# Kernel tuning notes

Measured on AMD Instinct MI355X. Metric: run time of the kernel, lower is better.

Reference implementation:

```python
import jax, jax.numpy as jnp
import numpy as np

B, N, CIN, COUT = 32, 2048, 64, 128
BN_EPS = 1e-5
ADJ_EPS = 1e-6


def setup_inputs() -> dict:
    key = jax.random.key(0)
    k0, k1, k2 = jax.random.split(key, 3)
    x = jax.random.normal(k0, (B, N, CIN), dtype=jnp.float32)
    # adjacency: nonnegative weights, like an attention/affinity graph
    A = jax.random.uniform(k1, (B, N, N), dtype=jnp.float32)
    # 1x1 conv == pointwise linear over channels
    W = jax.random.normal(k2, (COUT, CIN), dtype=jnp.float32) * 0.05
    b = jnp.zeros((COUT,), dtype=jnp.float32)
    gamma = jnp.ones((COUT,), dtype=jnp.float32)
    beta = jnp.zeros((COUT,), dtype=jnp.float32)
    return {"x": x, "A": A, "W": W, "b": b, "gamma": gamma, "beta": beta}


def reference(x, A, W, b, gamma, beta):
    # Row-normalize each batch adjacency: A[i] / (A[i].sum(dim=1, keepdim=True) + eps)
    A_norm = A / (jnp.sum(A, axis=2, keepdims=True) + ADJ_EPS)  # [B,N,N]
    # Batched graph aggregation: xg[b,c,m] = sum_n x[b,n,c] * A_norm[b,n,m]
    xg = jnp.einsum('bnc,bnm->bcm', x, A_norm)  # [B,C,N]
    # 1x1 conv (pointwise channel mix)
    h = jnp.einsum('bcm,oc->bom', xg, W) + b[None, :, None]  # [B,COUT,N]
    # BatchNorm2d in training mode: batch stats over (B, spatial) per channel,
    # biased variance (as PyTorch uses for normalization)
    mean = jnp.mean(h, axis=(0, 2), keepdims=True)
    var = jnp.mean((h - mean) ** 2, axis=(0, 2), keepdims=True)
    hn = (h - mean) * jax.lax.rsqrt(var + BN_EPS)
    hn = hn * gamma[None, :, None] + beta[None, :, None]
    out = jax.nn.relu(hn)
    # permute(0,2,1,3).squeeze(-1) -> [B, N, COUT]
    return jnp.transpose(out, (0, 2, 1))
```

## Files before the change

### kernel.cpp

```cpp
#include <hip/hip_runtime.h>

#define NB   32
#define NN   2048
#define CIN  64
#define COUT 128
#define ADJ_EPS 1e-6f
#define BN_EPS  1e-5f

typedef __attribute__((ext_vector_type(8))) short short8;
typedef __attribute__((ext_vector_type(4))) float floatx4;

#define BN1_OFF 0
#define BN2_OFF 128
#define SC_OFF  256
#define SH_OFF  384
#define XST_OFF 512

static __device__ __forceinline__ ushort f2bf(float f) {
    union { float f; unsigned u; } v; v.f = f;
    unsigned r = v.u + 0x7FFFu + ((v.u >> 16) & 1u);
    return (ushort)(r >> 16);
}
static __device__ __forceinline__ float bf2f(ushort u) {
    return __uint_as_float(((unsigned)u) << 16);
}

__global__ __launch_bounds__(256) void k1_norm(const float* __restrict__ A,
                                               const float* __restrict__ x,
                                               ushort* __restrict__ xsT) {
    __shared__ float invr[128];
    __shared__ __align__(16) ushort xsb[64 * 136];
    int b  = blockIdx.x & 31;
    int n0 = (blockIdx.x >> 5) * 128;
    int t  = threadIdx.x;
    int w  = t >> 6, lane = t & 63;

    for (int i = 0; i < 32; i += 2) {
        int r0 = w * 32 + i;
        const float4* a0 = (const float4*)(A + ((size_t)b * NN + n0 + r0) * NN);
        const float4* a1 = (const float4*)(A + ((size_t)b * NN + n0 + r0 + 1) * NN);
        float s0 = 0.f, s1 = 0.f;
#pragma unroll
        for (int j = 0; j < 8; ++j) {
            float4 v0 = a0[j * 64 + lane];
            float4 v1 = a1[j * 64 + lane];
            s0 += (v0.x + v0.y) + (v0.z + v0.w);
            s1 += (v1.x + v1.y) + (v1.z + v1.w);
        }
#pragma unroll
        for (int off = 32; off; off >>= 1) {
            s0 += __shfl_down(s0, off);
            s1 += __shfl_down(s1, off);
        }
        if (lane == 0) {
            invr[r0]     = 1.f / (s0 + ADJ_EPS);
            invr[r0 + 1] = 1.f / (s1 + ADJ_EPS);
        }
    }
    __syncthreads();
    {
        int c = t & 63, nh = t >> 6;
#pragma unroll
        for (int i = 0; i < 16; ++i) {
            int dn = nh * 32 + i * 2;
            float x0 = x[((size_t)b * NN + n0 + dn) * CIN + c] * invr[dn];
            float x1 = x[((size_t)b * NN + n0 + dn + 1) * CIN + c] * invr[dn + 1];
            ushort2 p; p.x = f2bf(x0); p.y = f2bf(x1);
            *(ushort2*)&xsb[c * 136 + dn] = p;
        }
    }
    __syncthreads();
    {
        int c = t >> 2, s = t & 3;
#pragma unroll
        for (int i = 0; i < 4; ++i) {
            short8 v = *(const short8*)&xsb[c * 136 + (s * 4 + i) * 8];
            *(short8*)&xsT[((size_t)b * CIN + c) * NN + n0 + (s * 4 + i) * 8] = v;
        }
    }
}

__global__ __launch_bounds__(256, 2) void k2_gemm(const float* __restrict__ A,
                                                  const ushort* __restrict__ xsT,
                                                  const float* __restrict__ W,
                                                  const float* __restrict__ bias,
                                                  float* __restrict__ hout,
                                                  float* __restrict__ bnsum,
                                                  float* __restrict__ bnsumsq) {
    __shared__ __align__(16) ushort Att[128 * 72];
    __shared__ __align__(16) ushort Xst[64 * 72];
    __shared__ __align__(16) float  xg[64 * 128];
    __shared__ __align__(16) ushort2 Wb[32 * 128];
    __shared__ float bn1[256], bn2[256];

    int b  = blockIdx.x & 31;
    int m0 = (blockIdx.x >> 5) * 128;
    int t  = threadIdx.x;
    int w  = t >> 6, lane = t & 63;
    int l15 = lane & 15, q = lane >> 4;

    {
        ushort* wbu = (ushort*)Wb;
        int c = t & 63, o0 = (t >> 6) * 32;
#pragma unroll
        for (int p = 0; p < 32; ++p) {
            int o = o0 + p;
            wbu[(c >> 1) * 256 + o * 2 + (c & 1)] = f2bf(W[o * CIN + c]);
        }
    }

    floatx4 acc[4][2];
#pragma unroll
    for (int ct = 0; ct < 4; ++ct)
#pragma unroll
        for (int j = 0; j < 2; ++j) {
            floatx4 z = {0.f, 0.f, 0.f, 0.f};
            acc[ct][j] = z;
        }

    for (int n0 = 0; n0 < NN; n0 += 64) {
        __syncthreads();
        {
            int mm = t & 127, nh = t >> 7;
            const float* Ab = A + ((size_t)b * NN + n0) * NN + m0 + mm;
#pragma unroll
            for (int i = 0; i < 16; ++i) {
                int dn = nh * 32 + i * 2;
                float a0 = Ab[(size_t)dn * NN];
                float a1 = Ab[(size_t)(dn + 1) * NN];
                ushort2 p; p.x = f2bf(a0); p.y = f2bf(a1);
                *(ushort2*)&Att[mm * 72 + dn] = p;
            }
        }
        {
            int c = t >> 2, s = t & 3;
#pragma unroll
            for (int i = 0; i < 2; ++i) {
                short8 v = *(const short8*)&xsT[((size_t)b * CIN + c) * NN + n0 + (s * 2 + i) * 8];
                *(short8*)&Xst[c * 72 + (s * 2 + i) * 8] = v;
            }
        }
        __syncthreads();
#pragma unroll
        for (int kk = 0; kk < 64; kk += 32) {
            short8 af[4], bfr[2];
#pragma unroll
            for (int ct = 0; ct < 4; ++ct)
                af[ct] = *(const short8*)&Xst[(ct * 16 + l15) * 72 + kk + q * 8];
#pragma unroll
            for (int j = 0; j < 2; ++j)
                bfr[j] = *(const short8*)&Att[((w * 2 + j) * 16 + l15) * 72 + kk + q * 8];
#pragma unroll
            for (int ct = 0; ct < 4; ++ct)
#pragma unroll
                for (int j = 0; j < 2; ++j)
                    acc[ct][j] = __builtin_amdgcn_mfma_f32_16x16x32_bf16(
                        af[ct], bfr[j], acc[ct][j], 0, 0, 0);
        }
    }
    __syncthreads();
#pragma unroll
    for (int ct = 0; ct < 4; ++ct)
#pragma unroll
        for (int j = 0; j < 2; ++j) {
            int col = (w * 2 + j) * 16 + l15;
#pragma unroll
            for (int r = 0; r < 4; ++r)
                xg[(ct * 16 + q * 4 + r) * 128 + col] = acc[ct][j][r];
        }
    __syncthreads();

    int o  = t & 127;
    int mq = t >> 7;
    float bo = bias[o];
    float s1 = 0.f, s2 = 0.f;
    for (int mc = 0; mc < 4; ++mc) {
        float h[16];
#pragma unroll
        for (int i = 0; i < 16; ++i) h[i] = bo;
#pragma unroll
        for (int c2 = 0; c2 < 32; ++c2) {
            ushort2 wp = Wb[c2 * 128 + o];
            float w0 = bf2f(wp.x), w1 = bf2f(wp.y);
            const float* x0p = &xg[(2 * c2) * 128 + mq * 64 + mc * 16];
            const float* x1p = &xg[(2 * c2 + 1) * 128 + mq * 64 + mc * 16];
#pragma unroll
            for (int v = 0; v < 4; ++v) {
                float4 g0 = *(const float4*)&x0p[v * 4];
                float4 g1 = *(const float4*)&x1p[v * 4];
                h[v * 4 + 0] = fmaf(w0, g0.x, fmaf(w1, g1.x, h[v * 4 + 0]));
                h[v * 4 + 1] = fmaf(w0, g0.y, fmaf(w1, g1.y, h[v * 4 + 1]));
                h[v * 4 + 2] = fmaf(w0, g0.z, fmaf(w1, g1.z, h[v * 4 + 2]));
                h[v * 4 + 3] = fmaf(w0, g0.w, fmaf(w1, g1.w, h[v * 4 + 3]));
            }
        }
        size_t base = ((size_t)b * NN + m0 + mq * 64 + mc * 16) * COUT + o;
#pragma unroll
        for (int i = 0; i < 16; ++i) {
            float v = h[i];
            s1 += v;
            s2 = fmaf(v, v, s2);
            hout[base + (size_t)i * COUT] = v;
        }
    }
    bn1[t] = s1;
    bn2[t] = s2;
    __syncthreads();
    if (t < 128) {
        atomicAdd(&bnsum[o],   bn1[t] + bn1[t + 128]);
        atomicAdd(&bnsumsq[o], bn2[t] + bn2[t + 128]);
    }
}

__global__ void k3_bnstats(const float* __restrict__ bnsum,
                           const float* __restrict__ bnsumsq,
                           const float* __restrict__ gamma,
                           const float* __restrict__ beta,
                           float* __restrict__ scale,
                           float* __restrict__ shift) {
    int o = threadIdx.x;
    if (o < COUT) {
        const float invn = 1.f / ((float)NB * (float)NN);
        float mean = bnsum[o] * invn;
        float var  = bnsumsq[o] * invn - mean * mean;
        float sc   = gamma[o] * rsqrtf(var + BN_EPS);
        scale[o] = sc;
        shift[o] = beta[o] - mean * sc;
    }
}

__global__ __launch_bounds__(256) void k4_bnapply(float* __restrict__ hout,
                                                  const float* __restrict__ scale,
                                                  const float* __restrict__ shift) {
    const float4* sc4 = (const float4*)scale;
    const float4* sh4 = (const float4*)shift;
    float4* h4 = (float4*)hout;
    const size_t n4 = (size_t)NB * NN * COUT / 4;
    for (size_t idx = (size_t)blockIdx.x * blockDim.x + threadIdx.x; idx < n4;
         idx += (size_t)gridDim.x * blockDim.x) {
        int o4 = (int)(idx & 31);
        float4 h = h4[idx];
        float4 s = sc4[o4];
        float4 f = sh4[o4];
        h.x = fmaxf(fmaf(h.x, s.x, f.x), 0.f);
        h.y = fmaxf(fmaf(h.y, s.y, f.y), 0.f);
        h.z = fmaxf(fmaf(h.z, s.z, f.z), 0.f);
        h.w = fmaxf(fmaf(h.w, s.w, f.w), 0.f);
        h4[idx] = h;
    }
}

extern "C" void kernel_launch(void* const* d_in, const int* in_sizes, int n_in,
                              void* d_out, int out_size, void* d_ws, size_t ws_size,
                              hipStream_t stream) {
    const float* x     = (const float*)d_in[0];
    const float* A     = (const float*)d_in[1];
    const float* W     = (const float*)d_in[2];
    const float* bvec  = (const float*)d_in[3];
    const float* gamma = (const float*)d_in[4];
    const float* beta  = (const float*)d_in[5];
    float* out = (float*)d_out;
    float* ws  = (float*)d_ws;

    float*  bnsum   = ws + BN1_OFF;
    float*  bnsumsq = ws + BN2_OFF;
    float*  scale   = ws + SC_OFF;
    float*  shift   = ws + SH_OFF;
    ushort* xsT     = (ushort*)(ws + XST_OFF);

    hipMemsetAsync(bnsum, 0, 256 * sizeof(float), stream);

    k1_norm<<<NB * (NN / 128), 256, 0, stream>>>(A, x, xsT);
    k2_gemm<<<NB * (NN / 128), 256, 0, stream>>>(A, xsT, W, bvec, out, bnsum, bnsumsq);
    k3_bnstats<<<1, 128, 0, stream>>>(bnsum, bnsumsq, gamma, beta, scale, shift);
    k4_bnapply<<<2048, 256, 0, stream>>>(out, scale, shift);
}
```

Measured before the change: 829.3 us.

## Pre-convert A to swizzled bf16 tiles and double-buffer GEMM loads via LDS DMA

The prep kernel now reads A once, computing row sums and writing a bf16, transposed, XOR-swizzled tiled copy of A to workspace. The GEMM kernel streams these pre-packed tiles and xsT straight into LDS with global_load_lds, double-buffered across the K loop, in place of strided fp32 loads with in-kernel conversion. This removes the second fp32 read of A and the uncoalesced column gathers. The cost is an extra bf16 write and read of A (256 MB of workspace) and a larger shared-memory footprint.

```diff
diff --git a/kernel.cpp b/kernel.cpp
--- a/kernel.cpp
+++ b/kernel.cpp
@@ -15,6 +15,7 @@
 #define SC_OFF  256
 #define SH_OFF  384
 #define XST_OFF 512
+#define ATT_OFF (512 + 2097152)
 
 static __device__ __forceinline__ ushort f2bf(float f) {
     union { float f; unsigned u; } v; v.f = f;
@@ -25,73 +26,116 @@
     return __uint_as_float(((unsigned)u) << 16);
 }
 
-__global__ __launch_bounds__(256) void k1_norm(const float* __restrict__ A,
-                                               const float* __restrict__ x,
-                                               ushort* __restrict__ xsT) {
-    __shared__ float invr[128];
-    __shared__ __align__(16) ushort xsb[64 * 136];
+static __device__ __forceinline__ void gload16(const void* g, void* l) {
+    __builtin_amdgcn_global_load_lds(
+        (const __attribute__((address_space(1))) unsigned int*)g,
+        (__attribute__((address_space(3))) unsigned int*)l, 16, 0, 0);
+}
+
+__global__ __launch_bounds__(256, 4) void k1_prep(const float* __restrict__ A,
+                                                  const float* __restrict__ x,
+                                                  ushort* __restrict__ xsT,
+                                                  ushort* __restrict__ ATt) {
+    __shared__ __align__(16) ushort ldsT[128 * 72];
+    __shared__ float invr[64];
     int b  = blockIdx.x & 31;
-    int n0 = (blockIdx.x >> 5) * 128;
+    int nt = blockIdx.x >> 5;
+    int n0 = nt * 64;
     int t  = threadIdx.x;
-    int w  = t >> 6, lane = t & 63;
-
-    for (int i = 0; i < 32; i += 2) {
-        int r0 = w * 32 + i;
-        const float4* a0 = (const float4*)(A + ((size_t)b * NN + n0 + r0) * NN);
-        const float4* a1 = (const float4*)(A + ((size_t)b * NN + n0 + r0 + 1) * NN);
-        float s0 = 0.f, s1 = 0.f;
-#pragma unroll
-        for (int j = 0; j < 8; ++j) {
-            float4 v0 = a0[j * 64 + lane];
-            float4 v1 = a1[j * 64 + lane];
-            s0 += (v0.x + v0.y) + (v0.z + v0.w);
-            s1 += (v1.x + v1.y) + (v1.z + v1.w);
-        }
-#pragma unroll
-        for (int off = 32; off; off >>= 1) {
-            s0 += __shfl_down(s0, off);
-            s1 += __shfl_down(s1, off);
-        }
-        if (lane == 0) {
-            invr[r0]     = 1.f / (s0 + ADJ_EPS);
-            invr[r0 + 1] = 1.f / (s1 + ADJ_EPS);
-        }
+    int c4 = t & 31, r8 = t >> 5;
+
+    float racc[8];
+#pragma unroll
+    for (int i = 0; i < 8; ++i) racc[i] = 0.f;
+
+    const float* Abase = A + ((size_t)b * NN + n0) * NN;
+    int isw = (c4 & 7);
+
+    for (int mc = 0; mc < 16; ++mc) {
+        int m0 = mc * 128;
+#pragma unroll
+        for (int p = 0; p < 4; ++p) {
+            int ra = r8 * 8 + 2 * p;
+            float4 va = *(const float4*)(Abase + (size_t)ra * NN + m0 + c4 * 4);
+            float4 vb = *(const float4*)(Abase + (size_t)(ra + 1) * NN + m0 + c4 * 4);
+            racc[2 * p]     += (va.x + va.y) + (va.z + va.w);
+            racc[2 * p + 1] += (vb.x + vb.y) + (vb.z + vb.w);
+            int gsw = (r8 ^ isw) * 8 + 2 * p;
+            ushort2 q0; q0.x = f2bf(va.x); q0.y = f2bf(vb.x);
+            ushort2 q1; q1.x = f2bf(va.y); q1.y = f2bf(vb.y);
+            ushort2 q2; q2.x = f2bf(va.z); q2.y = f2bf(vb.z);
+            ushort2 q3; q3.x = f2bf(va.w); q3.y = f2bf(vb.w);
+            *(ushort2*)&ldsT[(c4 * 4 + 0) * 72 + gsw] = q0;
+            *(ushort2*)&ldsT[(c4 * 4 + 1) * 72 + gsw] = q1;
+            *(ushort2*)&ldsT[(c4 * 4 + 2) * 72 + gsw] = q2;
+            *(ushort2*)&ldsT[(c4 * 4 + 3) * 72 + gsw] = q3;
+        }
+        __syncthreads();
+        {
+            int m = t >> 1, h = t & 1;
+            size_t obase = (((size_t)b * 32 + nt) * NN + m0 + m) * 64;
+            int msw = (m >> 2) & 7;
+#pragma unroll
+            for (int s = 0; s < 4; ++s) {
+                int slot  = h * 4 + s;
+                int gdata = slot ^ (m & 7);
+                int gpos  = gdata ^ msw;
+                short8 v = *(const short8*)&ldsT[m * 72 + gpos * 8];
+                *(short8*)&ATt[obase + slot * 8] = v;
+            }
+        }
+        __syncthreads();
+    }
+
+#pragma unroll
+    for (int i = 0; i < 8; ++i) {
+#pragma unroll
+        for (int off = 16; off; off >>= 1)
+            racc[i] += __shfl_xor(racc[i], off);
+    }
+    if (c4 == 0) {
+#pragma unroll
+        for (int i = 0; i < 8; ++i)
+            invr[r8 * 8 + i] = 1.f / (racc[i] + ADJ_EPS);
     }
     __syncthreads();
     {
-        int c = t & 63, nh = t >> 6;
+        int c = t & 63, nq = t >> 6;
 #pragma unroll
         for (int i = 0; i < 16; ++i) {
-            int dn = nh * 32 + i * 2;
-            float x0 = x[((size_t)b * NN + n0 + dn) * CIN + c] * invr[dn];
-            float x1 = x[((size_t)b * NN + n0 + dn + 1) * CIN + c] * invr[dn + 1];
-            ushort2 p; p.x = f2bf(x0); p.y = f2bf(x1);
-            *(ushort2*)&xsb[c * 136 + dn] = p;
-        }
-    }
-    __syncthreads();
-    {
-        int c = t >> 2, s = t & 3;
-#pragma unroll
-        for (int i = 0; i < 4; ++i) {
-            short8 v = *(const short8*)&xsb[c * 136 + (s * 4 + i) * 8];
-            *(short8*)&xsT[((size_t)b * CIN + c) * NN + n0 + (s * 4 + i) * 8] = v;
-        }
-    }
-}
-
-__global__ __launch_bounds__(256, 2) void k2_gemm(const float* __restrict__ A,
+            int n = nq * 16 + i;
+            float v = x[((size_t)b * NN + n0 + n) * CIN + c] * invr[n];
+            ldsT[c * 72 + n] = f2bf(v);
+        }
+    }
+    __syncthreads();
+    if (t < 128) {
+        int c = t >> 1, h = t & 1;
+        size_t obase = ((size_t)b * CIN + c) * NN + n0;
+#pragma unroll
+        for (int s = 0; s < 4; ++s) {
+            int slot  = h * 4 + s;
+            int gdata = slot ^ (c & 7);
+            short8 v = *(const short8*)&ldsT[c * 72 + gdata * 8];
+            *(short8*)&xsT[obase + slot * 8] = v;
+        }
+    }
+}
+
+__global__ __launch_bounds__(256, 2) void k2_gemm(const ushort* __restrict__ ATt,
                                                   const ushort* __restrict__ xsT,
                                                   const float* __restrict__ W,
                                                   const float* __restrict__ bias,
                                                   float* __restrict__ hout,
                                                   float* __restrict__ bnsum,
                                                   float* __restrict__ bnsumsq) {
-    __shared__ __align__(16) ushort Att[128 * 72];
-    __shared__ __align__(16) ushort Xst[64 * 72];
-    __shared__ __align__(16) float  xg[64 * 128];
-    __shared__ __align__(16) ushort2 Wb[32 * 128];
-    __shared__ float bn1[256], bn2[256];
+    __shared__ __align__(16) char smem[67584];
+    ushort* AttB = (ushort*)smem;
+    ushort* XstB = (ushort*)(smem + 32768);
+    float*  xg   = (float*)smem;
+    ushort* wbu  = (ushort*)(smem + 49152);
+    float*  bn1  = (float*)(smem + 65536);
+    float*  bn2  = bn1 + 256;
 
     int b  = blockIdx.x & 31;
     int m0 = (blockIdx.x >> 5) * 128;
@@ -100,7 +144,6 @@
     int l15 = lane & 15, q = lane >> 4;
 
     {
-        ushort* wbu = (ushort*)Wb;
         int c = t & 63, o0 = (t >> 6) * 32;
 #pragma unroll
         for (int p = 0; p < 32; ++p) {
@@ -109,6 +152,23 @@
         }
     }
 
+    const ushort* Asrc = ATt + ((size_t)b * 32 * NN + m0) * 64;
+    const ushort* Xsrc = xsT + (size_t)b * CIN * NN;
+
+    auto stage = [&](int nt, int buf) {
+        const ushort* ga = Asrc + (size_t)nt * (NN * 64);
+        ushort* la = AttB + buf * 8192;
+#pragma unroll
+        for (int r = 0; r < 4; ++r)
+            gload16(ga + (r * 256 + t) * 8, la + (r * 256 + t) * 8);
+        ushort* lx = XstB + buf * 4096;
+#pragma unroll
+        for (int r = 0; r < 2; ++r) {
+            int c = (r * 256 + t) >> 3, g = t & 7;
+            gload16(Xsrc + (size_t)c * NN + nt * 64 + g * 8, lx + c * 64 + g * 8);
+        }
+    };
+
     floatx4 acc[4][2];
 #pragma unroll
     for (int ct = 0; ct < 4; ++ct)
@@ -118,38 +178,29 @@
             acc[ct][j] = z;
         }
 
-    for (int n0 = 0; n0 < NN; n0 += 64) {
-        __syncthreads();
-        {
-            int mm = t & 127, nh = t >> 7;
-            const float* Ab = A + ((size_t)b * NN + n0) * NN + m0 + mm;
-#pragma unroll
-            for (int i = 0; i < 16; ++i) {
-                int dn = nh * 32 + i * 2;
-                float a0 = Ab[(size_t)dn * NN];
-                float a1 = Ab[(size_t)(dn + 1) * NN];
-                ushort2 p; p.x = f2bf(a0); p.y = f2bf(a1);
-                *(ushort2*)&Att[mm * 72 + dn] = p;
+    stage(0, 0);
+    __syncthreads();
+
+    for (int nt = 0; nt < 32; ++nt) {
+        int cur = nt & 1;
+        if (nt + 1 < 32) stage(nt + 1, cur ^ 1);
+        const ushort* la = AttB + cur * 8192;
+        const ushort* lx = XstB + cur * 4096;
+#pragma unroll
+        for (int kh = 0; kh < 2; ++kh) {
+            short8 af[4], bfr[2];
+#pragma unroll
+            for (int ct = 0; ct < 4; ++ct) {
+                int row  = ct * 16 + l15;
+                int slot = (kh * 4 + q) ^ (row & 7);
+                af[ct] = *(const short8*)&lx[row * 64 + slot * 8];
             }
-        }
-        {
-            int c = t >> 2, s = t & 3;
-#pragma unroll
-            for (int i = 0; i < 2; ++i) {
-                short8 v = *(const short8*)&xsT[((size_t)b * CIN + c) * NN + n0 + (s * 2 + i) * 8];
-                *(short8*)&Xst[c * 72 + (s * 2 + i) * 8] = v;
+#pragma unroll
+            for (int j = 0; j < 2; ++j) {
+                int row  = (w * 2 + j) * 16 + l15;
+                int slot = (kh * 4 + q) ^ (row & 7);
+                bfr[j] = *(const short8*)&la[row * 64 + slot * 8];
             }
-        }
-        __syncthreads();
-#pragma unroll
-        for (int kk = 0; kk < 64; kk += 32) {
-            short8 af[4], bfr[2];
-#pragma unroll
-            for (int ct = 0; ct < 4; ++ct)
-                af[ct] = *(const short8*)&Xst[(ct * 16 + l15) * 72 + kk + q * 8];
-#pragma unroll
-            for (int j = 0; j < 2; ++j)
-                bfr[j] = *(const short8*)&Att[((w * 2 + j) * 16 + l15) * 72 + kk + q * 8];
 #pragma unroll
             for (int ct = 0; ct < 4; ++ct)
 #pragma unroll
@@ -157,8 +208,9 @@
                     acc[ct][j] = __builtin_amdgcn_mfma_f32_16x16x32_bf16(
                         af[ct], bfr[j], acc[ct][j], 0, 0, 0);
         }
-    }
-    __syncthreads();
+        __syncthreads();
+    }
+
 #pragma unroll
     for (int ct = 0; ct < 4; ++ct)
 #pragma unroll
@@ -174,13 +226,14 @@
     int mq = t >> 7;
     float bo = bias[o];
     float s1 = 0.f, s2 = 0.f;
+    const ushort2* Wb2 = (const ushort2*)wbu;
     for (int mc = 0; mc < 4; ++mc) {
         float h[16];
 #pragma unroll
         for (int i = 0; i < 16; ++i) h[i] = bo;
 #pragma unroll
         for (int c2 = 0; c2 < 32; ++c2) {
-            ushort2 wp = Wb[c2 * 128 + o];
+            ushort2 wp = Wb2[c2 * 128 + o];
             float w0 = bf2f(wp.x), w1 = bf2f(wp.y);
             const float* x0p = &xg[(2 * c2) * 128 + mq * 64 + mc * 16];
             const float* x1p = &xg[(2 * c2 + 1) * 128 + mq * 64 + mc * 16];
@@ -267,11 +320,12 @@
     float*  scale   = ws + SC_OFF;
     float*  shift   = ws + SH_OFF;
     ushort* xsT     = (ushort*)(ws + XST_OFF);
+    ushort* ATt     = (ushort*)(ws + ATT_OFF);
 
     hipMemsetAsync(bnsum, 0, 256 * sizeof(float), stream);
 
-    k1_norm<<<NB * (NN / 128), 256, 0, stream>>>(A, x, xsT);
-    k2_gemm<<<NB * (NN / 128), 256, 0, stream>>>(A, xsT, W, bvec, out, bnsum, bnsumsq);
+    k1_prep<<<NB * (NN / 64), 256, 0, stream>>>(A, x, xsT, ATt);
+    k2_gemm<<<NB * (NN / 128), 256, 0, stream>>>(ATt, xsT, W, bvec, out, bnsum, bnsumsq);
     k3_bnstats<<<1, 128, 0, stream>>>(bnsum, bnsumsq, gamma, beta, scale, shift);
     k4_bnapply<<<2048, 256, 0, stream>>>(out, scale, shift);
 }
```

New measurement: 893.8 us. +7.8%, slower.
